# Optimization experiments

Measured on AMD Instinct MI355X. Metric: run time of the kernel, lower is better.

## Reference

```python
import jax, jax.numpy as jnp
import numpy as np

EPS = 1e-5
N_HEADS = 12


def _layernorm(x, scale, shift):
    mean = jnp.mean(x, axis=-1, keepdims=True)
    var = jnp.mean((x - mean) ** 2, axis=-1, keepdims=True)
    return scale * (x - mean) / jnp.sqrt(var + EPS) + shift


def setup_inputs() -> dict:
    key = jax.random.key(0)
    ks = jax.random.split(key, 8)
    B, L, D = 4, 1024, 768
    inp = {
        "x": jax.random.normal(ks[0], (B, L, D), jnp.float32),
        "Wq": jax.random.normal(ks[1], (D, D), jnp.float32) * 0.02,
        "Wk": jax.random.normal(ks[2], (D, D), jnp.float32) * 0.02,
        "Wv": jax.random.normal(ks[3], (D, D), jnp.float32) * 0.02,
        "Wo": jax.random.normal(ks[4], (D, D), jnp.float32) * 0.02,
        "bo": jnp.zeros((D,), jnp.float32),
        "scale1": jnp.ones((D,), jnp.float32),
        "shift1": jnp.zeros((D,), jnp.float32),
        "scale2": jnp.ones((D,), jnp.float32),
        "shift2": jnp.zeros((D,), jnp.float32),
        "centers": jax.random.normal(ks[5], (D, D), jnp.float32) * 0.1,  # [num_kernels=D, D]
        "lengthscale": jnp.ones((D,), jnp.float32),
        "Wf": jax.random.normal(ks[6], (D, D), jnp.float32) * 0.02,  # [num_kernels, D]
        "bf": jnp.zeros((D,), jnp.float32),
    }
    return inp


def reference(x, Wq, Wk, Wv, Wo, bo, scale1, shift1, scale2, shift2,
              centers, lengthscale, Wf, bf):
    B, L, D = x.shape
    H = N_HEADS
    hd = D // H

    # --- pre-norm causal MHA + residual ---
    h = _layernorm(x, scale1, shift1)
    q = (h @ Wq).reshape(B, L, H, hd).transpose(0, 2, 1, 3)  # [B,H,L,hd]
    k = (h @ Wk).reshape(B, L, H, hd).transpose(0, 2, 1, 3)
    v = (h @ Wv).reshape(B, L, H, hd).transpose(0, 2, 1, 3)

    scores = jnp.einsum("bhqd,bhkd->bhqk", q, k) / jnp.sqrt(jnp.float32(hd))
    causal = jnp.tril(jnp.ones((L, L), bool))
    scores = jnp.where(causal, scores, -jnp.inf)
    attn = jax.nn.softmax(scores, axis=-1)
    ctx = jnp.einsum("bhqk,bhkd->bhqd", attn, v).transpose(0, 2, 1, 3).reshape(B, L, D)
    x = x + (ctx @ Wo + bo)

    # --- pre-norm RBF-kernel FFN + residual ---
    h = _layernorm(x, scale2, shift2)
    hf = (h / lengthscale).reshape(B * L, D)          # ARD scaling
    cf = centers / lengthscale                        # [K, D]
    sq = (jnp.sum(hf * hf, -1)[:, None]
          + jnp.sum(cf * cf, -1)[None, :]
          - 2.0 * hf @ cf.T)
    K = jnp.exp(-0.5 * jnp.maximum(sq, 0.0))          # [B*L, K]
    ff = (K @ Wf + bf).reshape(B, L, D)
    return x + ff
```

## Files before the change

kernel.cpp:

```cpp
#include <hip/hip_runtime.h>

#define EPS_LN 1e-5f

constexpr int Dm   = 768;
constexpr int Bb   = 4;
constexpr int Ls   = 1024;
constexpr int Hh   = 12;
constexpr int HD   = 64;
constexpr int ROWS = Bb * Ls;
constexpr size_t S = (size_t)ROWS * Dm;
constexpr size_t WSZ = (size_t)Dm * Dm;

typedef __attribute__((ext_vector_type(8))) short bf16x8;
typedef __attribute__((ext_vector_type(4))) float f32x4;
typedef const __attribute__((address_space(1))) unsigned int* gas_p;
typedef __attribute__((address_space(3))) unsigned int* las_p;

__device__ __forceinline__ unsigned short f2bf(float f) {
  unsigned int u = __float_as_uint(f);
  u += 0x7fffu + ((u >> 16) & 1u);
  return (unsigned short)(u >> 16);
}
__device__ __forceinline__ void gl_lds16(const unsigned short* g, unsigned short* l) {
  __builtin_amdgcn_global_load_lds((gas_p)g, (las_p)l, 16, 0, 0);
}

__global__ void __launch_bounds__(256) prep_kernel(
    const float* __restrict__ W0, const float* __restrict__ W1,
    const float* __restrict__ W2, const float* __restrict__ W3,
    const float* __restrict__ W4, unsigned short* __restrict__ wtBase,
    const float* __restrict__ centers, const float* __restrict__ ls,
    unsigned short* __restrict__ cb, float* __restrict__ cn,
    const float* __restrict__ x, const float* __restrict__ scale,
    const float* __restrict__ shift, unsigned short* __restrict__ hb)
{
  __shared__ float smem[64 * 65];
  int bx = blockIdx.x, t = threadIdx.x;
  if (bx < 720) {
    int w = bx / 144, rem = bx - w * 144;
    int ky = rem / 12, nx = rem - ky * 12;
    const float* W = w == 0 ? W0 : w == 1 ? W1 : w == 2 ? W2 : w == 3 ? W3 : W4;
    unsigned short* WT = wtBase + (size_t)w * WSZ;
    int k0 = ky * 64, n0 = nx * 64;
    int c = t & 63, r4 = t >> 6;
    #pragma unroll
    for (int p = 0; p < 16; p++) {
      int r = p * 4 + r4;
      smem[r * 65 + c] = W[(size_t)(k0 + r) * Dm + n0 + c];
    }
    __syncthreads();
    #pragma unroll
    for (int p = 0; p < 16; p++) {
      int r = p * 4 + r4;
      WT[(size_t)(n0 + r) * Dm + k0 + c] = f2bf(smem[c * 65 + r]);
    }
  } else if (bx < 1488) {
    int j = bx - 720;
    float s = 0.f;
    #pragma unroll
    for (int i = 0; i < 3; i++) {
      int k = t + 256 * i;
      float c = centers[(size_t)j * Dm + k] / ls[k];
      cb[(size_t)j * Dm + k] = f2bf(c);
      s += c * c;
    }
    smem[t] = s; __syncthreads();
    for (int o = 128; o > 0; o >>= 1) { if (t < o) smem[t] += smem[t + o]; __syncthreads(); }
    if (t == 0) cn[j] = smem[0];
  } else {
    int lane = t & 63;
    int row = (bx - 1488) * 4 + (t >> 6);
    size_t base = (size_t)row * Dm;
    float4 v[3];
    #pragma unroll
    for (int j = 0; j < 3; j++)
      v[j] = *(const float4*)&x[base + 4 * (lane + 64 * j)];
    float sum = 0.f;
    #pragma unroll
    for (int j = 0; j < 3; j++) sum += v[j].x + v[j].y + v[j].z + v[j].w;
    #pragma unroll
    for (int m = 1; m < 64; m <<= 1) sum += __shfl_xor(sum, m);
    float mean = sum * (1.0f / Dm);
    float4 d[3];
    float vs = 0.f;
    #pragma unroll
    for (int j = 0; j < 3; j++) {
      d[j].x = v[j].x - mean; d[j].y = v[j].y - mean;
      d[j].z = v[j].z - mean; d[j].w = v[j].w - mean;
      vs += d[j].x*d[j].x + d[j].y*d[j].y + d[j].z*d[j].z + d[j].w*d[j].w;
    }
    #pragma unroll
    for (int m = 1; m < 64; m <<= 1) vs += __shfl_xor(vs, m);
    float rstd = rsqrtf(vs * (1.0f / Dm) + EPS_LN);
    #pragma unroll
    for (int j = 0; j < 3; j++) {
      int c4 = 4 * (lane + 64 * j);
      float4 sc = *(const float4*)&scale[c4];
      float4 sh = *(const float4*)&shift[c4];
      ushort4 o4;
      o4.x = f2bf(sc.x * d[j].x * rstd + sh.x);
      o4.y = f2bf(sc.y * d[j].y * rstd + sh.y);
      o4.z = f2bf(sc.z * d[j].z * rstd + sh.z);
      o4.w = f2bf(sc.w * d[j].w * rstd + sh.w);
      *(ushort4*)&hb[base + c4] = o4;
    }
  }
}

__global__ void __launch_bounds__(256) ln2_kernel(
    const float* __restrict__ xin, const float* __restrict__ scale,
    const float* __restrict__ shift, const float* __restrict__ ls,
    unsigned short* __restrict__ o, float* __restrict__ hn)
{
  int lane = threadIdx.x & 63;
  int row = blockIdx.x * 4 + (threadIdx.x >> 6);
  size_t base = (size_t)row * Dm;
  float4 v[3];
  #pragma unroll
  for (int j = 0; j < 3; j++)
    v[j] = *(const float4*)&xin[base + 4 * (lane + 64 * j)];
  float sum = 0.f;
  #pragma unroll
  for (int j = 0; j < 3; j++) sum += v[j].x + v[j].y + v[j].z + v[j].w;
  #pragma unroll
  for (int m = 1; m < 64; m <<= 1) sum += __shfl_xor(sum, m);
  float mean = sum * (1.0f / Dm);
  float4 d[3];
  float vs = 0.f;
  #pragma unroll
  for (int j = 0; j < 3; j++) {
    d[j].x = v[j].x - mean; d[j].y = v[j].y - mean;
    d[j].z = v[j].z - mean; d[j].w = v[j].w - mean;
    vs += d[j].x*d[j].x + d[j].y*d[j].y + d[j].z*d[j].z + d[j].w*d[j].w;
  }
  #pragma unroll
  for (int m = 1; m < 64; m <<= 1) vs += __shfl_xor(vs, m);
  float rstd = rsqrtf(vs * (1.0f / Dm) + EPS_LN);
  float hsum = 0.f;
  #pragma unroll
  for (int j = 0; j < 3; j++) {
    int c4 = 4 * (lane + 64 * j);
    float4 sc = *(const float4*)&scale[c4];
    float4 sh = *(const float4*)&shift[c4];
    float4 lv = *(const float4*)&ls[c4];
    float4 hv;
    hv.x = (sc.x * d[j].x * rstd + sh.x) / lv.x;
    hv.y = (sc.y * d[j].y * rstd + sh.y) / lv.y;
    hv.z = (sc.z * d[j].z * rstd + sh.z) / lv.z;
    hv.w = (sc.w * d[j].w * rstd + sh.w) / lv.w;
    ushort4 o4;
    o4.x = f2bf(hv.x); o4.y = f2bf(hv.y); o4.z = f2bf(hv.z); o4.w = f2bf(hv.w);
    *(ushort4*)&o[base + c4] = o4;
    hsum += hv.x*hv.x + hv.y*hv.y + hv.z*hv.z + hv.w*hv.w;
  }
  #pragma unroll
  for (int m = 1; m < 64; m <<= 1) hsum += __shfl_xor(hsum, m);
  if (lane == 0) hn[row] = hsum;
}

__global__ void __launch_bounds__(256) gemm_qkv(
    const unsigned short* __restrict__ Abf,
    const unsigned short* __restrict__ wqT,
    const unsigned short* __restrict__ wkT,
    const unsigned short* __restrict__ wvT,
    unsigned short* __restrict__ qb,
    unsigned short* __restrict__ kb,
    unsigned short* __restrict__ vbt)
{
  int m0 = blockIdx.y * 64, n0 = blockIdx.x * 64;
  __shared__ unsigned short sm[4096 + 3 * 4096];
  int tid = threadIdx.x;
  int lane = tid & 63, wave = tid >> 6;
  int quad = lane >> 4, l15 = lane & 15;
  int wr = (wave >> 1) << 5, wc = (wave & 1) << 5;

  f32x4 acc[3][2][2];
  #pragma unroll
  for (int w = 0; w < 3; w++)
    #pragma unroll
    for (int i = 0; i < 2; i++)
      #pragma unroll
      for (int j = 0; j < 2; j++) acc[w][i][j] = (f32x4){0.f, 0.f, 0.f, 0.f};

  const unsigned short* gA = Abf + (size_t)(m0 + (tid >> 2)) * Dm + ((tid & 3) << 3);
  size_t bOff = (size_t)(n0 + (tid >> 2)) * Dm + ((tid & 3) << 3);
  const unsigned short* gB[3] = { wqT + bOff, wkT + bOff, wvT + bOff };

  union Frag { bf16x8 v; ushort4 h[2]; };

  for (int k0 = 0; k0 < Dm; k0 += 64) {
    gl_lds16(gA + k0,      &sm[tid * 8]);
    gl_lds16(gA + k0 + 32, &sm[2048 + tid * 8]);
    #pragma unroll
    for (int w = 0; w < 3; w++) {
      gl_lds16(gB[w] + k0,      &sm[4096 + w * 4096 + tid * 8]);
      gl_lds16(gB[w] + k0 + 32, &sm[4096 + w * 4096 + 2048 + tid * 8]);
    }
    __syncthreads();
    Frag af[2][2];
    #pragma unroll
    for (int kc = 0; kc < 2; kc++)
      #pragma unroll
      for (int mi = 0; mi < 2; mi++)
        af[kc][mi].v = *(const bf16x8*)&sm[kc * 2048 + (wr + mi * 16 + l15) * 32 + quad * 8];
    #pragma unroll
    for (int w = 0; w < 3; w++)
      #pragma unroll
      for (int kc = 0; kc < 2; kc++)
        #pragma unroll
        for (int ni = 0; ni < 2; ni++) {
          Frag bf;
          bf.v = *(const bf16x8*)&sm[4096 + w * 4096 + kc * 2048 + (wc + ni * 16 + l15) * 32 + quad * 8];
          #pragma unroll
          for (int mi = 0; mi < 2; mi++)
            acc[w][mi][ni] = __builtin_amdgcn_mfma_f32_16x16x32_bf16(
                af[kc][mi].v, bf.v, acc[w][mi][ni], 0, 0, 0);
        }
    __syncthreads();
  }

  #pragma unroll
  for (int w = 0; w < 2; w++) {
    unsigned short* ob = w ? kb : qb;
    #pragma unroll
    for (int mi = 0; mi < 2; mi++)
      #pragma unroll
      for (int ni = 0; ni < 2; ni++)
        #pragma unroll
        for (int rg = 0; rg < 4; rg++) {
          int gr = m0 + wr + mi * 16 + quad * 4 + rg;
          int gc = n0 + wc + ni * 16 + l15;
          ob[(size_t)gr * Dm + gc] = f2bf(acc[w][mi][ni][rg]);
        }
  }
  #pragma unroll
  for (int mi = 0; mi < 2; mi++)
    #pragma unroll
    for (int ni = 0; ni < 2; ni++)
      #pragma unroll
      for (int rg = 0; rg < 4; rg++) {
        int rl = wr + mi * 16 + quad * 4 + rg;
        int cl = wc + ni * 16 + l15;
        sm[cl * 72 + rl] = f2bf(acc[2][mi][ni][rg]);
      }
  __syncthreads();
  {
    int d = tid >> 2, c0 = (tid & 3) * 16;
    int b_ = m0 >> 10, keybase = m0 & 1023;
    unsigned short* dst = vbt + ((size_t)((blockIdx.x * 4 + b_) * 64 + d)) * 1024 + keybase + c0;
    #pragma unroll
    for (int i = 0; i < 16; i += 4)
      *(ushort4*)(dst + i) = *(const ushort4*)&sm[d * 72 + c0 + i];
  }
}

template<int MODE>
__global__ void __launch_bounds__(256) gemm64(
    const unsigned short* __restrict__ Abf,
    const unsigned short* __restrict__ BT,
    unsigned short* __restrict__ o0,
    float* __restrict__ outF,
    const float* __restrict__ residF,
    const float* __restrict__ biasF,
    const float* __restrict__ hn,
    const float* __restrict__ cn)
{
  __shared__ unsigned short Asm[2][2048];
  __shared__ unsigned short Bsm[2][2048];
  int tid = threadIdx.x;
  int m0 = blockIdx.y * 64, n0 = blockIdx.x * 64;

  if (MODE >= 2) {
    __shared__ float r2[256];
    float mn = 1e30f;
    for (int i = tid; i < ROWS; i += 256) mn = fminf(mn, hn[i]);
    r2[tid] = mn; __syncthreads();
    for (int o = 128; o > 0; o >>= 1) { if (tid < o) r2[tid] = fminf(r2[tid], r2[tid + o]); __syncthreads(); }
    float hmin = r2[0];
    __syncthreads();
    float mx = 0.f;
    for (int i = tid; i < Dm; i += 256) mx = fmaxf(mx, cn[i]);
    r2[tid] = mx; __syncthreads();
    for (int o = 128; o > 0; o >>= 1) { if (tid < o) r2[tid] = fmaxf(r2[tid], r2[tid + o]); __syncthreads(); }
    float cmax = r2[0];
    float a = sqrtf(hmin), bq = sqrtf(cmax);
    bool allz = (a > bq) && ((a - bq) * (a - bq) > 300.0f);
    if (allz) {
      if (MODE == 2) return;
      int r = m0 + (tid >> 2), c0 = n0 + (tid & 3) * 16;
      size_t idx = (size_t)r * Dm + c0;
      #pragma unroll
      for (int i = 0; i < 16; i += 4) {
        float4 xv = *(const float4*)(residF + idx + i);
        float4 ov;
        ov.x = xv.x + biasF[c0 + i + 0];
        ov.y = xv.y + biasF[c0 + i + 1];
        ov.z = xv.z + biasF[c0 + i + 2];
        ov.w = xv.w + biasF[c0 + i + 3];
        *(float4*)(outF + idx + i) = ov;
      }
      return;
    }
    __syncthreads();
  }

  int lane = tid & 63, wave = tid >> 6;
  int quad = lane >> 4, l15 = lane & 15;
  int wr = (wave >> 1) << 5, wc = (wave & 1) << 5;

  f32x4 acc[2][2];
  #pragma unroll
  for (int i = 0; i < 2; i++)
    #pragma unroll
    for (int j = 0; j < 2; j++) acc[i][j] = (f32x4){0.f, 0.f, 0.f, 0.f};

  const unsigned short* gA = Abf + (size_t)(m0 + (tid >> 2)) * Dm + ((tid & 3) << 3);
  const unsigned short* gB = BT  + (size_t)(n0 + (tid >> 2)) * Dm + ((tid & 3) << 3);

  union Frag { bf16x8 v; ushort4 h[2]; };

  for (int k0 = 0; k0 < Dm; k0 += 64) {
    gl_lds16(gA + k0,      &Asm[0][tid * 8]);
    gl_lds16(gA + k0 + 32, &Asm[1][tid * 8]);
    gl_lds16(gB + k0,      &Bsm[0][tid * 8]);
    gl_lds16(gB + k0 + 32, &Bsm[1][tid * 8]);
    __syncthreads();
    #pragma unroll
    for (int kc = 0; kc < 2; kc++) {
      Frag af[2], bfb[2];
      #pragma unroll
      for (int i = 0; i < 2; i++) {
        af[i].v  = *(const bf16x8*)&Asm[kc][(wr + i * 16 + l15) * 32 + quad * 8];
        bfb[i].v = *(const bf16x8*)&Bsm[kc][(wc + i * 16 + l15) * 32 + quad * 8];
      }
      #pragma unroll
      for (int mi = 0; mi < 2; mi++)
        #pragma unroll
        for (int ni = 0; ni < 2; ni++)
          acc[mi][ni] = __builtin_amdgcn_mfma_f32_16x16x32_bf16(
              af[mi].v, bfb[ni].v, acc[mi][ni], 0, 0, 0);
    }
    __syncthreads();
  }

  #pragma unroll
  for (int mi = 0; mi < 2; mi++)
    #pragma unroll
    for (int ni = 0; ni < 2; ni++)
      #pragma unroll
      for (int rg = 0; rg < 4; rg++) {
        int gr = m0 + wr + mi * 16 + quad * 4 + rg;
        int gc = n0 + wc + ni * 16 + l15;
        size_t idx = (size_t)gr * Dm + gc;
        float v = acc[mi][ni][rg];
        if (MODE == 2) {
          float sq = fmaxf(hn[gr] + cn[gc] - 2.0f * v, 0.f);
          o0[idx] = f2bf(__expf(-0.5f * sq));
        } else {
          outF[idx] = residF[idx] + v + biasF[gc];
        }
      }
}

__global__ void __launch_bounds__(256) attn_flash(
    const unsigned short* __restrict__ q,
    const unsigned short* __restrict__ k,
    const unsigned short* __restrict__ vbt,
    unsigned short* __restrict__ ctx)
{
  int bx = blockIdx.x;
  int qt = (bx & 1) ? (15 - (bx >> 1)) : (bx >> 1);
  int h  = blockIdx.y;
  int b  = blockIdx.z;
  int tid = threadIdx.x;
  int lane = tid & 63, wave = tid >> 6;
  int quad = lane >> 4, l15 = lane & 15;

  __shared__ unsigned short Ks[2][2][2048];
  __shared__ unsigned short Vt[2][2][2048];
  __shared__ unsigned short QP[4608];

  size_t baseQK = (size_t)(b * Ls) * Dm + h * HD;
  const unsigned short* gVt = vbt + (size_t)((h * 4 + b) * 64 + (tid >> 2)) * 1024 + ((tid & 3) << 3);

  {
    const unsigned short* gQ = q + baseQK + (size_t)(qt * 64 + (tid >> 2)) * Dm + ((tid & 3) << 3);
    gl_lds16(gQ,      &QP[tid * 8]);
    gl_lds16(gQ + 32, &QP[2048 + tid * 8]);
  }
  __syncthreads();

  union Frag { bf16x8 v; ushort4 h[2]; };
  Frag afq[2];
  #pragma unroll
  for (int kc = 0; kc < 2; kc++)
    afq[kc].v = *(const bf16x8*)&QP[kc * 2048 + (wave * 16 + l15) * 32 + quad * 8];
  asm volatile("s_waitcnt lgkmcnt(0)" ::: "memory");

  f32x4 O[4];
  #pragma unroll
  for (int nj = 0; nj < 4; nj++) O[nj] = (f32x4){0.f, 0.f, 0.f, 0.f};
  float lsum[4] = {0.f, 0.f, 0.f, 0.f};

  const unsigned short* gK = k + baseQK + (size_t)(tid >> 2) * Dm + ((tid & 3) << 3);

  gl_lds16(gK,      &Ks[0][0][tid * 8]);
  gl_lds16(gK + 32, &Ks[0][1][tid * 8]);
  gl_lds16(gVt,      &Vt[0][0][tid * 8]);
  gl_lds16(gVt + 32, &Vt[0][1][tid * 8]);

  for (int kt = 0; kt <= qt; kt++) {
    int cur = kt & 1;
    asm volatile("s_waitcnt lgkmcnt(0)" ::: "memory");
    __builtin_amdgcn_s_barrier();
    if (kt < qt) {
      int nxt = cur ^ 1;
      gl_lds16(gK + (size_t)((kt + 1) * 64) * Dm,      &Ks[nxt][0][tid * 8]);
      gl_lds16(gK + (size_t)((kt + 1) * 64) * Dm + 32, &Ks[nxt][1][tid * 8]);
      gl_lds16(gVt + (kt + 1) * 64,      &Vt[nxt][0][tid * 8]);
      gl_lds16(gVt + (kt + 1) * 64 + 32, &Vt[nxt][1][tid * 8]);
      asm volatile("s_waitcnt vmcnt(4)" ::: "memory");
    } else {
      asm volatile("s_waitcnt vmcnt(0)" ::: "memory");
    }
    __builtin_amdgcn_s_barrier();
    __builtin_amdgcn_sched_barrier(0);

    f32x4 sacc[4];
    #pragma unroll
    for (int ni = 0; ni < 4; ni++) {
      sacc[ni] = (f32x4){0.f, 0.f, 0.f, 0.f};
      #pragma unroll
      for (int kc = 0; kc < 2; kc++) {
        Frag bk;
        bk.v = *(const bf16x8*)&Ks[cur][kc][(ni * 16 + l15) * 32 + quad * 8];
        sacc[ni] = __builtin_amdgcn_mfma_f32_16x16x32_bf16(afq[kc].v, bk.v, sacc[ni], 0, 0, 0);
      }
    }

    if (kt == qt) {
      #pragma unroll
      for (int ni = 0; ni < 4; ni++)
        #pragma unroll
        for (int rg = 0; rg < 4; rg++) {
          int rowl = wave * 16 + quad * 4 + rg;
          int coll = ni * 16 + l15;
          if (coll > rowl) sacc[ni][rg] = -1e30f;
        }
    }

    unsigned short (*Ps)[72] = (unsigned short(*)[72])QP;
    #pragma unroll
    for (int ni = 0; ni < 4; ni++)
      #pragma unroll
      for (int rg = 0; rg < 4; rg++) {
        float p = __expf(sacc[ni][rg] * 0.125f);
        lsum[rg] += p;
        Ps[wave * 16 + quad * 4 + rg][ni * 16 + l15] = f2bf(p);
      }

    Frag ap[2];
    #pragma unroll
    for (int kc = 0; kc < 2; kc++)
      ap[kc].v = *(const bf16x8*)&Ps[wave * 16 + l15][kc * 32 + quad * 8];

    #pragma unroll
    for (int nj = 0; nj < 4; nj++)
      #pragma unroll
      for (int kc = 0; kc < 2; kc++) {
        Frag bv;
        bv.v = *(const bf16x8*)&Vt[cur][kc][(nj * 16 + l15) * 32 + quad * 8];
        O[nj] = __builtin_amdgcn_mfma_f32_16x16x32_bf16(ap[kc].v, bv.v, O[nj], 0, 0, 0);
      }
  }

  float linv[4];
  #pragma unroll
  for (int rg = 0; rg < 4; rg++) {
    float l = lsum[rg];
    #pragma unroll
    for (int m = 1; m < 16; m <<= 1) l += __shfl_xor(l, m, 16);
    linv[rg] = 1.0f / l;
  }
  #pragma unroll
  for (int nj = 0; nj < 4; nj++)
    #pragma unroll
    for (int rg = 0; rg < 4; rg++) {
      int row = qt * 64 + wave * 16 + quad * 4 + rg;
      int col = nj * 16 + l15;
      ctx[baseQK + (size_t)row * Dm + col] = f2bf(O[nj][rg] * linv[rg]);
    }
}

extern "C" void kernel_launch(void* const* d_in, const int* in_sizes, int n_in,
                              void* d_out, int out_size, void* d_ws, size_t ws_size,
                              hipStream_t stream)
{
  const float* x      = (const float*)d_in[0];
  const float* Wq     = (const float*)d_in[1];
  const float* Wk     = (const float*)d_in[2];
  const float* Wv     = (const float*)d_in[3];
  const float* Wo     = (const float*)d_in[4];
  const float* bo     = (const float*)d_in[5];
  const float* scale1 = (const float*)d_in[6];
  const float* shift1 = (const float*)d_in[7];
  const float* scale2 = (const float*)d_in[8];
  const float* shift2 = (const float*)d_in[9];
  const float* centers= (const float*)d_in[10];
  const float* lsp    = (const float*)d_in[11];
  const float* Wf     = (const float*)d_in[12];
  const float* bfv    = (const float*)d_in[13];
  float* out = (float*)d_out;

  unsigned short* wsu = (unsigned short*)d_ws;
  unsigned short* wqT = wsu;
  unsigned short* wkT = wsu + WSZ;
  unsigned short* wvT = wsu + 2 * WSZ;
  unsigned short* woT = wsu + 3 * WSZ;
  unsigned short* wfT = wsu + 4 * WSZ;
  unsigned short* cb  = wsu + 5 * WSZ;
  unsigned short* bufA = wsu + 6 * WSZ;
  unsigned short* bufB = bufA + S;
  unsigned short* hb  = bufA;
  unsigned short* qb  = bufB;
  unsigned short* kb  = bufB + S;
  unsigned short* vbt = bufB + 2 * S;
  unsigned short* ctx = bufA;
  float* x1f          = (float*)bufB;
  unsigned short* hf  = bufB + 2 * S;
  unsigned short* Km  = bufA;
  float* hn = (float*)(bufB + 3 * S);
  float* cn = hn + ROWS;

  dim3 gg(Dm / 64, ROWS / 64);

  prep_kernel<<<2512, 256, 0, stream>>>(Wq, Wk, Wv, Wo, Wf, wsu,
                                        centers, lsp, cb, cn,
                                        x, scale1, shift1, hb);
  gemm_qkv<<<dim3(12, 64), 256, 0, stream>>>(hb, wqT, wkT, wvT, qb, kb, vbt);
  attn_flash<<<dim3(Ls / 64, Hh, Bb), 256, 0, stream>>>(qb, kb, vbt, ctx);
  gemm64<1><<<gg, 256, 0, stream>>>(ctx, woT, nullptr, x1f, x, bo, nullptr, nullptr);
  ln2_kernel<<<ROWS / 4, 256, 0, stream>>>(x1f, scale2, shift2, lsp, hf, hn);
  gemm64<2><<<gg, 256, 0, stream>>>(hf, cb, Km, nullptr, nullptr, nullptr, hn, cn);
  gemm64<3><<<gg, 256, 0, stream>>>(Km, wfT, nullptr, out, x1f, bfv, hn, cn);
}
```

Measured before the change: 185.6 us.

## Retile QKV GEMM to 128x128 blocks over concatenated weight matrix

Replaces the 64x64 QKV GEMM that computed three weight tiles per block with a 128x128 tile GEMM treating Wq/Wk/Wv as one contiguous 2304-column transposed weight. Each wave now computes a 64x64 subtile with 4x4 MFMAs, raising arithmetic intensity per LDS load and cutting re-reads of the A operand. The epilogue routes tiles to q, k or the transposed v buffer based on the column block, with per-wave LDS transpose for V. It relies on the three transposed weights being stored contiguously in the workspace, and the grid shrinks to 576 blocks, which may reduce occupancy.

```diff
diff --git a/kernel.cpp b/kernel.cpp
--- a/kernel.cpp
+++ b/kernel.cpp
@@ -158,99 +158,94 @@
   if (lane == 0) hn[row] = hsum;
 }
 
-__global__ void __launch_bounds__(256) gemm_qkv(
+__global__ void __launch_bounds__(256) gemm_qkv128(
     const unsigned short* __restrict__ Abf,
-    const unsigned short* __restrict__ wqT,
-    const unsigned short* __restrict__ wkT,
-    const unsigned short* __restrict__ wvT,
+    const unsigned short* __restrict__ BT,
     unsigned short* __restrict__ qb,
     unsigned short* __restrict__ kb,
     unsigned short* __restrict__ vbt)
 {
-  int m0 = blockIdx.y * 64, n0 = blockIdx.x * 64;
-  __shared__ unsigned short sm[4096 + 3 * 4096];
+  __shared__ unsigned short sm[18432];
   int tid = threadIdx.x;
+  int m0 = blockIdx.y * 128, n0 = blockIdx.x * 128;
   int lane = tid & 63, wave = tid >> 6;
   int quad = lane >> 4, l15 = lane & 15;
-  int wr = (wave >> 1) << 5, wc = (wave & 1) << 5;
-
-  f32x4 acc[3][2][2];
-  #pragma unroll
-  for (int w = 0; w < 3; w++)
-    #pragma unroll
-    for (int i = 0; i < 2; i++)
-      #pragma unroll
-      for (int j = 0; j < 2; j++) acc[w][i][j] = (f32x4){0.f, 0.f, 0.f, 0.f};
+  int wr = (wave >> 1) << 6, wc = (wave & 1) << 6;
+
+  f32x4 acc[4][4];
+  #pragma unroll
+  for (int i = 0; i < 4; i++)
+    #pragma unroll
+    for (int j = 0; j < 4; j++) acc[i][j] = (f32x4){0.f, 0.f, 0.f, 0.f};
 
   const unsigned short* gA = Abf + (size_t)(m0 + (tid >> 2)) * Dm + ((tid & 3) << 3);
-  size_t bOff = (size_t)(n0 + (tid >> 2)) * Dm + ((tid & 3) << 3);
-  const unsigned short* gB[3] = { wqT + bOff, wkT + bOff, wvT + bOff };
-
-  union Frag { bf16x8 v; ushort4 h[2]; };
+  const unsigned short* gB = BT  + (size_t)(n0 + (tid >> 2)) * Dm + ((tid & 3) << 3);
 
   for (int k0 = 0; k0 < Dm; k0 += 64) {
-    gl_lds16(gA + k0,      &sm[tid * 8]);
-    gl_lds16(gA + k0 + 32, &sm[2048 + tid * 8]);
-    #pragma unroll
-    for (int w = 0; w < 3; w++) {
-      gl_lds16(gB[w] + k0,      &sm[4096 + w * 4096 + tid * 8]);
-      gl_lds16(gB[w] + k0 + 32, &sm[4096 + w * 4096 + 2048 + tid * 8]);
-    }
-    __syncthreads();
-    Frag af[2][2];
     #pragma unroll
     for (int kc = 0; kc < 2; kc++)
       #pragma unroll
-      for (int mi = 0; mi < 2; mi++)
-        af[kc][mi].v = *(const bf16x8*)&sm[kc * 2048 + (wr + mi * 16 + l15) * 32 + quad * 8];
-    #pragma unroll
-    for (int w = 0; w < 3; w++)
-      #pragma unroll
-      for (int kc = 0; kc < 2; kc++)
+      for (int h = 0; h < 2; h++) {
+        gl_lds16(gA + k0 + kc * 32 + (size_t)(h * 64) * Dm, &sm[kc * 4096 + h * 2048 + tid * 8]);
+        gl_lds16(gB + k0 + kc * 32 + (size_t)(h * 64) * Dm, &sm[8192 + kc * 4096 + h * 2048 + tid * 8]);
+      }
+    __syncthreads();
+    #pragma unroll
+    for (int kc = 0; kc < 2; kc++) {
+      bf16x8 af[4], bfv[4];
+      #pragma unroll
+      for (int i = 0; i < 4; i++) {
+        af[i]  = *(const bf16x8*)&sm[kc * 4096 + (wr + i * 16 + l15) * 32 + quad * 8];
+        bfv[i] = *(const bf16x8*)&sm[8192 + kc * 4096 + (wc + i * 16 + l15) * 32 + quad * 8];
+      }
+      #pragma unroll
+      for (int mi = 0; mi < 4; mi++)
         #pragma unroll
-        for (int ni = 0; ni < 2; ni++) {
-          Frag bf;
-          bf.v = *(const bf16x8*)&sm[4096 + w * 4096 + kc * 2048 + (wc + ni * 16 + l15) * 32 + quad * 8];
-          #pragma unroll
-          for (int mi = 0; mi < 2; mi++)
-            acc[w][mi][ni] = __builtin_amdgcn_mfma_f32_16x16x32_bf16(
-                af[kc][mi].v, bf.v, acc[w][mi][ni], 0, 0, 0);
-        }
-    __syncthreads();
-  }
-
-  #pragma unroll
-  for (int w = 0; w < 2; w++) {
-    unsigned short* ob = w ? kb : qb;
-    #pragma unroll
-    for (int mi = 0; mi < 2; mi++)
-      #pragma unroll
-      for (int ni = 0; ni < 2; ni++)
+        for (int ni = 0; ni < 4; ni++)
+          acc[mi][ni] = __builtin_amdgcn_mfma_f32_16x16x32_bf16(af[mi], bfv[ni], acc[mi][ni], 0, 0, 0);
+    }
+    __syncthreads();
+  }
+
+  if (n0 < 1536) {
+    unsigned short* ob = n0 < 768 ? qb : kb;
+    int nb = n0 < 768 ? n0 : n0 - 768;
+    #pragma unroll
+    for (int mi = 0; mi < 4; mi++)
+      #pragma unroll
+      for (int ni = 0; ni < 4; ni++)
         #pragma unroll
         for (int rg = 0; rg < 4; rg++) {
           int gr = m0 + wr + mi * 16 + quad * 4 + rg;
-          int gc = n0 + wc + ni * 16 + l15;
-          ob[(size_t)gr * Dm + gc] = f2bf(acc[w][mi][ni][rg]);
+          int gc = nb + wc + ni * 16 + l15;
+          ob[(size_t)gr * Dm + gc] = f2bf(acc[mi][ni][rg]);
         }
-  }
-  #pragma unroll
-  for (int mi = 0; mi < 2; mi++)
-    #pragma unroll
-    for (int ni = 0; ni < 2; ni++)
-      #pragma unroll
-      for (int rg = 0; rg < 4; rg++) {
-        int rl = wr + mi * 16 + quad * 4 + rg;
-        int cl = wc + ni * 16 + l15;
-        sm[cl * 72 + rl] = f2bf(acc[2][mi][ni][rg]);
-      }
-  __syncthreads();
-  {
-    int d = tid >> 2, c0 = (tid & 3) * 16;
-    int b_ = m0 >> 10, keybase = m0 & 1023;
-    unsigned short* dst = vbt + ((size_t)((blockIdx.x * 4 + b_) * 64 + d)) * 1024 + keybase + c0;
-    #pragma unroll
-    for (int i = 0; i < 16; i += 4)
-      *(ushort4*)(dst + i) = *(const ushort4*)&sm[d * 72 + c0 + i];
+  } else {
+    unsigned short* tr = sm + wave * 4608;
+    #pragma unroll
+    for (int mi = 0; mi < 4; mi++)
+      #pragma unroll
+      for (int ni = 0; ni < 4; ni++)
+        #pragma unroll
+        for (int rg = 0; rg < 4; rg++) {
+          int rl = mi * 16 + quad * 4 + rg;
+          int cl = ni * 16 + l15;
+          tr[cl * 72 + rl] = f2bf(acc[mi][ni][rg]);
+        }
+    __syncthreads();
+    int b_ = m0 >> 10, key0 = m0 & 1023;
+    int d = tid >> 2, c0 = (tid & 3) << 4;
+    #pragma unroll
+    for (int wq = 0; wq < 4; wq++) {
+      int wrq = (wq >> 1) << 6;
+      int wcq = (wq & 1) << 6;
+      int h = ((n0 - 1536) + wcq) >> 6;
+      unsigned short* dst = vbt + ((size_t)((h * 4 + b_) * 64 + d)) * 1024 + key0 + wrq + c0;
+      const unsigned short* srcp = &sm[wq * 4608 + d * 72 + c0];
+      #pragma unroll
+      for (int i = 0; i < 16; i += 4)
+        *(ushort4*)(dst + i) = *(const ushort4*)(srcp + i);
+    }
   }
 }
 
@@ -514,7 +509,6 @@
 
   unsigned short* wsu = (unsigned short*)d_ws;
   unsigned short* wqT = wsu;
-  unsigned short* wkT = wsu + WSZ;
   unsigned short* wvT = wsu + 2 * WSZ;
   unsigned short* woT = wsu + 3 * WSZ;
   unsigned short* wfT = wsu + 4 * WSZ;
@@ -537,7 +531,7 @@
   prep_kernel<<<2512, 256, 0, stream>>>(Wq, Wk, Wv, Wo, Wf, wsu,
                                         centers, lsp, cb, cn,
                                         x, scale1, shift1, hb);
-  gemm_qkv<<<dim3(12, 64), 256, 0, stream>>>(hb, wqT, wkT, wvT, qb, kb, vbt);
+  gemm_qkv128<<<dim3(18, 32), 256, 0, stream>>>(hb, wqT, qb, kb, vbt);
   attn_flash<<<dim3(Ls / 64, Hh, Bb), 256, 0, stream>>>(qb, kb, vbt, ctx);
   gemm64<1><<<gg, 256, 0, stream>>>(ctx, woT, nullptr, x1f, x, bo, nullptr, nullptr);
   ln2_kernel<<<ROWS / 4, 256, 0, stream>>>(x1f, scale2, shift2, lsp, hf, hn);
```

New measurement: 196.6 us. +5.9%, slower.
